# Kernel tuning notes

Measured on AMD Instinct MI355X. Metric: run time of the kernel, lower is better.

Reference implementation:

```python
import jax, jax.numpy as jnp
import numpy as np

N = 100_000      # nodes
E = 1_600_000    # nonzeros of the rescaled Laplacian (avg degree 16)
F_IN = 128
F_OUT = 128
K = 4


def setup_inputs() -> dict:
    key = jax.random.key(0)
    ks = jax.random.split(key, 6)
    x = jax.random.normal(ks[0], (N, F_IN), dtype=jnp.float32)
    filter_coeff = jax.random.normal(ks[1], (K, N), dtype=jnp.float32)
    # glorot-ish scale for [K, F_in, F_out]
    stdv = float(np.sqrt(6.0 / (F_IN + F_OUT)))
    weight = jax.random.uniform(ks[2], (K, F_IN, F_OUT), dtype=jnp.float32,
                                minval=-stdv, maxval=stdv)
    bias = jnp.zeros((F_OUT,), dtype=jnp.float32)
    src = jax.random.randint(ks[3], (E,), 0, N, dtype=jnp.int32)
    dst = jax.random.randint(ks[4], (E,), 0, N, dtype=jnp.int32)
    # edge values of L_hat = 2L/lambda_max - I (precomputed sparse matrix)
    edge_w = jax.random.normal(ks[5], (E,), dtype=jnp.float32) * 0.1
    return {"x": x, "filter_coeff": filter_coeff, "weight": weight,
            "bias": bias, "edge_w": edge_w, "src": src, "dst": dst}


def reference(x, filter_coeff, weight, bias, edge_w, src, dst):
    n = x.shape[0]

    def spmm(h):  # edge-weighted gather-scale-segment_sum == dgl.update_all
        return jax.ops.segment_sum(h[src] * edge_w[:, None], dst,
                                   num_segments=n)

    # Chebyshev recurrence: T0 = x, T1 = L_hat x, T_k = 2 L_hat T_{k-1} - T_{k-2}
    Tx0 = x
    out = (filter_coeff[0][:, None] * Tx0) @ weight[0]
    Tx1 = spmm(x)
    out = out + (filter_coeff[1][:, None] * Tx1) @ weight[1]
    for k in range(2, weight.shape[0]):
        Tx2 = 2.0 * spmm(Tx1) - Tx0
        out = out + (filter_coeff[k][:, None] * Tx2) @ weight[k]
        Tx0, Tx1 = Tx1, Tx2
    return out + bias
```

## Files before the change

kernel.cpp:

```cpp
#include <hip/hip_runtime.h>
#include <hip/hip_bf16.h>
#include <cstdio>

#define F 128
#define BSHIFT 9
#define BROWS 512
#define C2 4096

typedef __attribute__((ext_vector_type(4))) float f32x4;
typedef __attribute__((ext_vector_type(4))) unsigned short u16x4;
typedef __attribute__((ext_vector_type(8))) short s16x8;

__device__ inline unsigned short f2bf(float x) {
  unsigned int u = __float_as_uint(x);
  u += 0x7fffu + ((u >> 16) & 1u);
  return (unsigned short)(u >> 16);
}
__device__ inline float bf2f(unsigned int h) {
  return __uint_as_float(h << 16);
}

__global__ void bucket_hist_kernel(const int* __restrict__ dst, int* __restrict__ bhist,
                                   int E, int B) {
  __shared__ int h[256];
  int t = threadIdx.x;
  h[t] = 0;
  __syncthreads();
  for (int e = blockIdx.x * blockDim.x + t; e < E; e += gridDim.x * blockDim.x)
    atomicAdd(&h[dst[e] >> BSHIFT], 1);
  __syncthreads();
  if (t < B && h[t]) atomicAdd(&bhist[t], h[t]);
}

__global__ void bucket_scan_kernel(const int* __restrict__ bhist, int* __restrict__ bbase,
                                   int* __restrict__ bcursor, int* __restrict__ rp,
                                   int E, int B, int N) {
  __shared__ int sm[256];
  int t = threadIdx.x;
  int v = (t < B) ? bhist[t] : 0;
  sm[t] = v;
  __syncthreads();
  int x = v;
  for (int off = 1; off < 256; off <<= 1) {
    int add = (t >= off) ? sm[t - off] : 0;
    __syncthreads();
    x += add;
    sm[t] = x;
    __syncthreads();
  }
  int excl = x - v;
  if (t < B) { bbase[t] = excl; bcursor[t] = excl; }
  if (t == 0) { bbase[B] = E; rp[N] = E; }
}

__global__ __launch_bounds__(256) void bucket_scatter_kernel(
    const int* __restrict__ src, const int* __restrict__ dst, const float* __restrict__ ew,
    int* __restrict__ bcursor, unsigned int* __restrict__ stg_p, float* __restrict__ stg_w,
    int E, int B) {
  __shared__ int hist[256], gbase[256], cur[256], sm[256], scn[256];
  __shared__ unsigned int sp[C2];
  __shared__ float swt[C2];
  __shared__ int sdest[C2];
  int t = threadIdx.x;
  int e0 = blockIdx.x * C2;
  int cnt = min(C2, E - e0);
  hist[t] = 0;
  __syncthreads();
#pragma unroll
  for (int i = 0; i < C2 / 256; ++i) {
    int e = e0 + t + i * 256;
    if (e < E) atomicAdd(&hist[dst[e] >> BSHIFT], 1);
  }
  __syncthreads();
  int v = hist[t];
  gbase[t] = (t < B && v) ? atomicAdd(&bcursor[t], v) : 0;
  sm[t] = v;
  __syncthreads();
  int x = v;
  for (int off = 1; off < 256; off <<= 1) {
    int add = (t >= off) ? sm[t - off] : 0;
    __syncthreads();
    x += add;
    sm[t] = x;
    __syncthreads();
  }
  scn[t] = x - v;
  cur[t] = 0;
  __syncthreads();
#pragma unroll
  for (int i = 0; i < C2 / 256; ++i) {
    int e = e0 + t + i * 256;
    if (e < E) {
      int d = dst[e];
      int b = d >> BSHIFT;
      int r = atomicAdd(&cur[b], 1);
      int slot = scn[b] + r;
      sp[slot] = (unsigned int)src[e] | ((unsigned int)(d & (BROWS - 1)) << 17);
      swt[slot] = ew[e];
      sdest[slot] = gbase[b] + r;
    }
  }
  __syncthreads();
#pragma unroll
  for (int i = 0; i < C2 / 256; ++i) {
    int s = t + i * 256;
    if (s < cnt) {
      int dpos = sdest[s];
      stg_p[dpos] = sp[s];
      stg_w[dpos] = swt[s];
    }
  }
}

__global__ __launch_bounds__(256) void csr_build_kernel(
    const unsigned int* __restrict__ stg_p, const float* __restrict__ stg_w,
    const int* __restrict__ bbase, int* __restrict__ rp, int2* __restrict__ csr,
    int N, int B) {
  __shared__ int rhist[BROWS], rloc[BROWS], curp[BROWS];
  __shared__ int sm[256];
  int b = blockIdx.x, t = threadIdx.x;
  int row0 = b << BSHIFT;
  int base = bbase[b];
  int cnt = bbase[b + 1] - base;
  rhist[t] = 0;
  rhist[t + 256] = 0;
  __syncthreads();
  for (int s = base + t; s < base + cnt; s += 256)
    atomicAdd(&rhist[stg_p[s] >> 17], 1);
  __syncthreads();
  int a0 = rhist[2 * t], a1 = rhist[2 * t + 1];
  int pv = a0 + a1;
  sm[t] = pv;
  __syncthreads();
  int x = pv;
  for (int off = 1; off < 256; off <<= 1) {
    int add = (t >= off) ? sm[t - off] : 0;
    __syncthreads();
    x += add;
    sm[t] = x;
    __syncthreads();
  }
  int pexcl = x - pv;
  int r0 = 2 * t, r1 = 2 * t + 1;
  rloc[r0] = pexcl;
  rloc[r1] = pexcl + a0;
  if (row0 + r0 < N) rp[row0 + r0] = base + rloc[r0];
  if (row0 + r1 < N) rp[row0 + r1] = base + rloc[r1];
  curp[r0] = base + rloc[r0];
  curp[r1] = base + rloc[r1];
  __syncthreads();
  for (int s = base + t; s < base + cnt; s += 256) {
    unsigned int p = stg_p[s];
    int dl = p >> 17;
    int pos = atomicAdd(&curp[dl], 1);
    int2 entry;
    entry.x = (int)(p & 0x1ffffu);
    entry.y = __float_as_int(stg_w[s]);
    csr[pos] = entry;
  }
}

__global__ void convx_kernel(const float* __restrict__ x, unsigned short* __restrict__ xbf,
                             int total4) {
  int i = blockIdx.x * 256 + threadIdx.x;
  if (i >= total4) return;
  f32x4 v = ((const f32x4*)x)[i];
  u16x4 o;
  o.x = f2bf(v.x); o.y = f2bf(v.y); o.z = f2bf(v.z); o.w = f2bf(v.w);
  ((u16x4*)xbf)[i] = o;
}

__global__ __launch_bounds__(256) void spmm_kernel(
    const unsigned short* __restrict__ Tin, const unsigned short* __restrict__ Tsub,
    unsigned short* __restrict__ Tout, const int* __restrict__ rp,
    const int2* __restrict__ csr, int n, float scale) {
  int wv = blockIdx.x * (blockDim.x >> 6) + (threadIdx.x >> 6);
  if (wv >= n) return;
  int lane = threadIdx.x & 63;
  int sl = lane & 15;
  int eo = lane >> 4;
  int j0 = rp[wv], end = rp[wv + 1];
  const uint4* Tin4 = (const uint4*)Tin;
  float acc[8];
#pragma unroll
  for (int c = 0; c < 8; ++c) acc[c] = 0.f;

  for (int j = j0; j < end; j += 16) {
    int2 e[4];
    float w[4];
    uint4 v[4];
#pragma unroll
    for (int u = 0; u < 4; ++u) {
      int je = j + 4 * u + eo;
      bool live = je < end;
      e[u] = csr[live ? je : end - 1];
      w[u] = live ? __int_as_float(e[u].y) : 0.f;
    }
#pragma unroll
    for (int u = 0; u < 4; ++u) v[u] = Tin4[(size_t)e[u].x * 16 + sl];
#pragma unroll
    for (int u = 0; u < 4; ++u) {
      acc[0] = fmaf(w[u], bf2f(v[u].x & 0xffffu), acc[0]);
      acc[1] = fmaf(w[u], bf2f(v[u].x >> 16), acc[1]);
      acc[2] = fmaf(w[u], bf2f(v[u].y & 0xffffu), acc[2]);
      acc[3] = fmaf(w[u], bf2f(v[u].y >> 16), acc[3]);
      acc[4] = fmaf(w[u], bf2f(v[u].z & 0xffffu), acc[4]);
      acc[5] = fmaf(w[u], bf2f(v[u].z >> 16), acc[5]);
      acc[6] = fmaf(w[u], bf2f(v[u].w & 0xffffu), acc[6]);
      acc[7] = fmaf(w[u], bf2f(v[u].w >> 16), acc[7]);
    }
  }
#pragma unroll
  for (int h = 16; h <= 32; h <<= 1)
#pragma unroll
    for (int c = 0; c < 8; ++c) acc[c] += __shfl_xor(acc[c], h, 64);

  if (eo == 0) {
    float r[8];
#pragma unroll
    for (int c = 0; c < 8; ++c) r[c] = scale * acc[c];
    if (Tsub) {
      uint4 p = ((const uint4*)Tsub)[(size_t)wv * 16 + sl];
      r[0] -= bf2f(p.x & 0xffffu); r[1] -= bf2f(p.x >> 16);
      r[2] -= bf2f(p.y & 0xffffu); r[3] -= bf2f(p.y >> 16);
      r[4] -= bf2f(p.z & 0xffffu); r[5] -= bf2f(p.z >> 16);
      r[6] -= bf2f(p.w & 0xffffu); r[7] -= bf2f(p.w >> 16);
    }
    uint4 o;
    o.x = (unsigned)f2bf(r[0]) | ((unsigned)f2bf(r[1]) << 16);
    o.y = (unsigned)f2bf(r[2]) | ((unsigned)f2bf(r[3]) << 16);
    o.z = (unsigned)f2bf(r[4]) | ((unsigned)f2bf(r[5]) << 16);
    o.w = (unsigned)f2bf(r[6]) | ((unsigned)f2bf(r[7]) << 16);
    ((uint4*)Tout)[(size_t)wv * 16 + sl] = o;
  }
}

__global__ void convw_kernel(const float* __restrict__ W, unsigned short* __restrict__ Wt,
                             int total, int Kd) {
  int idx = blockIdx.x * 256 + threadIdx.x;
  if (idx >= total) return;
  int nn = idx / Kd;
  int rem = idx - nn * Kd;
  int kk = rem >> 7;
  int r = rem & 127;
  Wt[idx] = f2bf(W[(size_t)kk * F * F + (size_t)r * F + nn]);
}

struct GemmArgs {
  const unsigned short* A[8];
  const float* fc;
  const unsigned short* Wt;
  const float* bias;
  float* out;
  int n;
  int kslices;
};

__global__ __launch_bounds__(256) void gemm_kernel(GemmArgs args) {
  __shared__ __align__(16) unsigned short lds_a[128][72];
  __shared__ __align__(16) unsigned short lds_b[128][72];
  const int t = threadIdx.x;
  const int lane = t & 63;
  const int wid = t >> 6;
  const int wrow = wid >> 1, wcol = wid & 1;
  const int bm = blockIdx.x * 128;
  const int n = args.n;
  const int kiters = args.kslices * 2;
  const int pitchW = args.kslices * 128;

  const int srow = t >> 4;
  const int scol = (t & 15) * 4;

  f32x4 acc[4][4];
#pragma unroll
  for (int a = 0; a < 4; ++a)
#pragma unroll
    for (int b = 0; b < 4; ++b) acc[a][b] = (f32x4){0.f, 0.f, 0.f, 0.f};

  for (int it = 0; it < kiters; ++it) {
    __syncthreads();
    const int ks = it >> 1;
    const unsigned short* As = args.A[ks];
    const float* fcs = args.fc + (size_t)ks * n;
    const int cbase = (it & 1) * 64 + scol;
#pragma unroll
    for (int i = 0; i < 8; ++i) {
      int r = srow + 16 * i;
      int rg = bm + r;
      int rc = rg < n ? rg : n - 1;
      u16x4 v = *(const u16x4*)(As + (size_t)rc * F + cbase);
      float f = fcs[rc];
      u16x4 sv;
      sv.x = f2bf(bf2f(v.x) * f);
      sv.y = f2bf(bf2f(v.y) * f);
      sv.z = f2bf(bf2f(v.z) * f);
      sv.w = f2bf(bf2f(v.w) * f);
      *(u16x4*)&lds_a[r][scol] = sv;
    }
    {
      const unsigned short* Ws = args.Wt + it * 64;
#pragma unroll
      for (int i = 0; i < 8; ++i) {
        int r = srow + 16 * i;
        u16x4 w = *(const u16x4*)(Ws + (size_t)r * pitchW + scol);
        *(u16x4*)&lds_b[r][scol] = w;
      }
    }
    __syncthreads();
#pragma unroll
    for (int kk = 0; kk < 2; ++kk) {
      s16x8 af[4], bfr[4];
#pragma unroll
      for (int mt = 0; mt < 4; ++mt)
        af[mt] = *(const s16x8*)&lds_a[wrow * 64 + mt * 16 + (lane & 15)][kk * 32 + (lane >> 4) * 8];
#pragma unroll
      for (int nt = 0; nt < 4; ++nt)
        bfr[nt] = *(const s16x8*)&lds_b[wcol * 64 + nt * 16 + (lane & 15)][kk * 32 + (lane >> 4) * 8];
#pragma unroll
      for (int mt = 0; mt < 4; ++mt)
#pragma unroll
        for (int nt = 0; nt < 4; ++nt)
          acc[mt][nt] = __builtin_amdgcn_mfma_f32_16x16x32_bf16(af[mt], bfr[nt], acc[mt][nt], 0, 0, 0);
    }
  }

#pragma unroll
  for (int nt = 0; nt < 4; ++nt) {
    int col = wcol * 64 + nt * 16 + (lane & 15);
    float bv = args.bias[col];
#pragma unroll
    for (int mt = 0; mt < 4; ++mt) {
#pragma unroll
      for (int r4 = 0; r4 < 4; ++r4) {
        int row = bm + wrow * 64 + mt * 16 + (lane >> 4) * 4 + r4;
        if (row < n) args.out[(size_t)row * F + col] = acc[mt][nt][r4] + bv;
      }
    }
  }
}

extern "C" void kernel_launch(void* const* d_in, const int* in_sizes, int n_in,
                              void* d_out, int out_size, void* d_ws, size_t ws_size,
                              hipStream_t stream) {
  const float* x    = (const float*)d_in[0];
  const float* fc   = (const float*)d_in[1];
  const float* W    = (const float*)d_in[2];
  const float* bias = (const float*)d_in[3];
  const float* ew   = (const float*)d_in[4];
  const int*   src  = (const int*)d_in[5];
  const int*   dst  = (const int*)d_in[6];

  const int N = in_sizes[0] / F;
  const int K = in_sizes[2] / (F * F);
  const int E = in_sizes[4];
  const int B = (N + BROWS - 1) >> BSHIFT;

  size_t off = 0;
  char* base = (char*)d_ws;
  auto alloc = [&](size_t bytes) -> void* {
    void* p = base + off;
    off += (bytes + 511) & ~(size_t)511;
    return p;
  };
  int* rp              = (int*)alloc(((size_t)N + 1) * 4);
  int* bhist           = (int*)alloc(1024);
  int* bbase           = (int*)alloc(1040);
  int* bcursor         = (int*)alloc(1024);
  int2* csr            = (int2*)alloc((size_t)E * 8);
  unsigned short* Wt   = (unsigned short*)alloc((size_t)K * F * F * 2);
  unsigned short* xbf  = (unsigned short*)alloc((size_t)N * F * 2);
  unsigned short* T[8];
  T[0] = xbf;
  for (int k = 1; k < K && k < 8; ++k) T[k] = (unsigned short*)alloc((size_t)N * F * 2);
  unsigned int* stg_p;
  float* stg_w;
  if (K >= 3 && (size_t)N * F * 2 >= (size_t)E * 8) {
    stg_p = (unsigned int*)T[2];
    stg_w = (float*)(T[2] + (size_t)E * 2);
  } else {
    stg_p = (unsigned int*)alloc((size_t)E * 4);
    stg_w = (float*)alloc((size_t)E * 4);
  }
  if (off > ws_size) {
    fprintf(stderr, "kernel_launch: ws too small: need %zu have %zu\n", off, ws_size);
    return;
  }

  hipMemsetAsync(bhist, 0, 1024, stream);
  int hblocks = (E + 255) / 256;
  if (hblocks > 2048) hblocks = 2048;
  hipLaunchKernelGGL(bucket_hist_kernel, dim3(hblocks), dim3(256), 0, stream, dst, bhist, E, B);
  hipLaunchKernelGGL(bucket_scan_kernel, dim3(1), dim3(256), 0, stream, bhist, bbase, bcursor,
                     rp, E, B, N);
  int sblocks = (E + C2 - 1) / C2;
  hipLaunchKernelGGL(bucket_scatter_kernel, dim3(sblocks), dim3(256), 0, stream, src, dst, ew,
                     bcursor, stg_p, stg_w, E, B);
  hipLaunchKernelGGL(csr_build_kernel, dim3(B), dim3(256), 0, stream, stg_p, stg_w, bbase,
                     rp, csr, N, B);

  int total4 = N * F / 4;
  hipLaunchKernelGGL(convx_kernel, dim3((total4 + 255) / 256), dim3(256), 0, stream,
                     x, xbf, total4);

  int sb = (N + 3) / 4;
  if (K > 1)
    hipLaunchKernelGGL(spmm_kernel, dim3(sb), dim3(256), 0, stream, xbf,
                       (const unsigned short*)nullptr, T[1], rp, csr, N, 1.0f);
  for (int k = 2; k < K; ++k) {
    const unsigned short* prev = T[k - 2];
    hipLaunchKernelGGL(spmm_kernel, dim3(sb), dim3(256), 0, stream, T[k - 1], prev, T[k],
                       rp, csr, N, 2.0f);
  }

  int total = K * F * F;
  hipLaunchKernelGGL(convw_kernel, dim3((total + 255) / 256), dim3(256), 0, stream, W, Wt,
                     total, K * F);

  GemmArgs ga;
  for (int k = 0; k < 8; ++k) ga.A[k] = (k < K) ? T[k] : xbf;
  ga.fc = fc; ga.Wt = Wt; ga.bias = bias;
  ga.out = (float*)d_out;
  ga.n = N; ga.kslices = K;
  hipLaunchKernelGGL(gemm_kernel, dim3((N + 127) / 128), dim3(256), 0, stream, ga);
}
```

Measured before the change: 354.3 us.

## Double-buffer GEMM A tiles via async global-to-LDS loads, apply filter coeff post-MFMA

Restructures the final GEMM kernel so each k-slice's full 128x128 bf16 A tile is loaded straight into XOR-swizzled LDS with global_load_lds, double-buffered so the next slice loads while the current one runs on MFMA. Weights are read directly from global memory into registers rather than staged through LDS. The per-row filter coefficient is now applied to the fp32 partial products after each slice instead of rescaling A in bf16 before the multiply. This removes the per-element convert-scale-convert work and the synchronous staging. In exchange it uses more LDS and registers (launch bounds now target 2 blocks per unit) and slightly changes rounding.

```diff
diff --git a/kernel.cpp b/kernel.cpp
--- a/kernel.cpp
+++ b/kernel.cpp
@@ -18,6 +18,12 @@
 }
 __device__ inline float bf2f(unsigned int h) {
   return __uint_as_float(h << 16);
+}
+
+__device__ inline void async_load16(const void* g, void* l) {
+  __builtin_amdgcn_global_load_lds(
+      (const __attribute__((address_space(1))) void*)g,
+      (__attribute__((address_space(3))) void*)l, 16, 0, 0);
 }
 
 __global__ void bucket_hist_kernel(const int* __restrict__ dst, int* __restrict__ bhist,
@@ -256,72 +262,109 @@
   int kslices;
 };
 
-__global__ __launch_bounds__(256) void gemm_kernel(GemmArgs args) {
-  __shared__ __align__(16) unsigned short lds_a[128][72];
-  __shared__ __align__(16) unsigned short lds_b[128][72];
+__global__ __launch_bounds__(256, 2) void gemm_kernel(GemmArgs args) {
+  __shared__ __align__(16) unsigned short Alds[2][128 * 128];
+  __shared__ float fcT[8][128];
   const int t = threadIdx.x;
   const int lane = t & 63;
   const int wid = t >> 6;
   const int wrow = wid >> 1, wcol = wid & 1;
   const int bm = blockIdx.x * 128;
   const int n = args.n;
-  const int kiters = args.kslices * 2;
-  const int pitchW = args.kslices * 128;
-
-  const int srow = t >> 4;
-  const int scol = (t & 15) * 4;
-
-  f32x4 acc[4][4];
+  const int KS = args.kslices;
+  const int pitchW = KS * 128;
+
+  for (int i = t; i < KS * 128; i += 256) {
+    int k = i >> 7, r = i & 127;
+    int rg = bm + r;
+    if (rg >= n) rg = n - 1;
+    fcT[k][r] = args.fc[(size_t)k * n + rg];
+  }
+  asm volatile("s_waitcnt lgkmcnt(0)" ::: "memory");
+
+  const int rloc = lane >> 4;
+  const int uu = lane & 15;
+  auto stageA = [&](int ks, int b) {
+    const unsigned short* As = args.A[ks];
+#pragma unroll
+    for (int i = 0; i < 8; ++i) {
+      int c = wid * 8 + i;
+      int row = c * 4 + rloc;
+      int rg = bm + row;
+      if (rg >= n) rg = n - 1;
+      const void* g = (const void*)(As + (size_t)rg * F + (size_t)((uu ^ (row & 7)) << 3));
+      void* l = (void*)(&Alds[b][0] + c * 512);
+      async_load16(g, l);
+    }
+  };
+
+  f32x4 Cf[4][4];
 #pragma unroll
   for (int a = 0; a < 4; ++a)
 #pragma unroll
-    for (int b = 0; b < 4; ++b) acc[a][b] = (f32x4){0.f, 0.f, 0.f, 0.f};
-
-  for (int it = 0; it < kiters; ++it) {
-    __syncthreads();
-    const int ks = it >> 1;
-    const unsigned short* As = args.A[ks];
-    const float* fcs = args.fc + (size_t)ks * n;
-    const int cbase = (it & 1) * 64 + scol;
-#pragma unroll
-    for (int i = 0; i < 8; ++i) {
-      int r = srow + 16 * i;
-      int rg = bm + r;
-      int rc = rg < n ? rg : n - 1;
-      u16x4 v = *(const u16x4*)(As + (size_t)rc * F + cbase);
-      float f = fcs[rc];
-      u16x4 sv;
-      sv.x = f2bf(bf2f(v.x) * f);
-      sv.y = f2bf(bf2f(v.y) * f);
-      sv.z = f2bf(bf2f(v.z) * f);
-      sv.w = f2bf(bf2f(v.w) * f);
-      *(u16x4*)&lds_a[r][scol] = sv;
-    }
-    {
-      const unsigned short* Ws = args.Wt + it * 64;
-#pragma unroll
-      for (int i = 0; i < 8; ++i) {
-        int r = srow + 16 * i;
-        u16x4 w = *(const u16x4*)(Ws + (size_t)r * pitchW + scol);
-        *(u16x4*)&lds_b[r][scol] = w;
+    for (int bq = 0; bq < 4; ++bq) Cf[a][bq] = (f32x4){0.f, 0.f, 0.f, 0.f};
+
+  stageA(0, 0);
+
+  const int arow_b = wrow * 64 + (lane & 15);
+  const int brow_b = wcol * 64 + (lane & 15);
+  const int ke = lane >> 4;
+
+  for (int ks = 0; ks < KS; ++ks) {
+    const int b = ks & 1;
+
+    s16x8 bfr[4][4];
+    const unsigned short* Wb = args.Wt + (size_t)brow_b * pitchW + ks * 128 + ke * 8;
+#pragma unroll
+    for (int nt = 0; nt < 4; ++nt)
+#pragma unroll
+      for (int kk = 0; kk < 4; ++kk)
+        bfr[nt][kk] = *(const s16x8*)(Wb + (size_t)(nt * 16) * pitchW + kk * 32);
+
+    if (ks + 1 < KS) {
+      stageA(ks + 1, b ^ 1);
+      asm volatile("s_waitcnt vmcnt(8)" ::: "memory");
+    } else {
+      asm volatile("s_waitcnt vmcnt(0)" ::: "memory");
+    }
+    __builtin_amdgcn_sched_barrier(0);
+    __builtin_amdgcn_s_barrier();
+    __builtin_amdgcn_sched_barrier(0);
+
+    f32x4 acc[4][4];
+#pragma unroll
+    for (int a = 0; a < 4; ++a)
+#pragma unroll
+      for (int bq = 0; bq < 4; ++bq) acc[a][bq] = (f32x4){0.f, 0.f, 0.f, 0.f};
+
+#pragma unroll
+    for (int kk = 0; kk < 4; ++kk) {
+      s16x8 afr[4];
+#pragma unroll
+      for (int mt = 0; mt < 4; ++mt) {
+        int row = arow_b + mt * 16;
+        int unit = (kk * 4 + ke) ^ (row & 7);
+        afr[mt] = *(const s16x8*)&Alds[b][row * F + (unit << 3)];
       }
-    }
-    __syncthreads();
-#pragma unroll
-    for (int kk = 0; kk < 2; ++kk) {
-      s16x8 af[4], bfr[4];
 #pragma unroll
       for (int mt = 0; mt < 4; ++mt)
-        af[mt] = *(const s16x8*)&lds_a[wrow * 64 + mt * 16 + (lane & 15)][kk * 32 + (lane >> 4) * 8];
+#pragma unroll
+        for (int nt = 0; nt < 4; ++nt)
+          acc[mt][nt] = __builtin_amdgcn_mfma_f32_16x16x32_bf16(afr[mt], bfr[nt][kk],
+                                                                acc[mt][nt], 0, 0, 0);
+    }
+
+#pragma unroll
+    for (int mt = 0; mt < 4; ++mt) {
+      f32x4 fv = *(const f32x4*)&fcT[ks][wrow * 64 + mt * 16 + (lane >> 4) * 4];
 #pragma unroll
       for (int nt = 0; nt < 4; ++nt)
-        bfr[nt] = *(const s16x8*)&lds_b[wcol * 64 + nt * 16 + (lane & 15)][kk * 32 + (lane >> 4) * 8];
-#pragma unroll
-      for (int mt = 0; mt < 4; ++mt)
-#pragma unroll
-        for (int nt = 0; nt < 4; ++nt)
-          acc[mt][nt] = __builtin_amdgcn_mfma_f32_16x16x32_bf16(af[mt], bfr[nt], acc[mt][nt], 0, 0, 0);
-    }
+        Cf[mt][nt] += fv * acc[mt][nt];
+    }
+
+    __builtin_amdgcn_sched_barrier(0);
+    __builtin_amdgcn_s_barrier();
+    __builtin_amdgcn_sched_barrier(0);
   }
 
 #pragma unroll
@@ -333,7 +376,7 @@
 #pragma unroll
       for (int r4 = 0; r4 < 4; ++r4) {
         int row = bm + wrow * 64 + mt * 16 + (lane >> 4) * 4 + r4;
-        if (row < n) args.out[(size_t)row * F + col] = acc[mt][nt][r4] + bv;
+        if (row < n) args.out[(size_t)row * F + col] = Cf[mt][nt][r4] + bv;
       }
     }
   }
```

Measured after the change: 360.6 us. Within noise of the previous version (+1.8%).

## Drop LDS staging in GEMM; apply filter coefficients post-MFMA per K-slice

Applied to the files above, without the earlier changes.

The GEMM no longer stages A and W tiles through shared memory with barriers. Each wave computes a 32x128 output block, loading A fragments directly from global memory and W from a pre-permuted fragment-order layout built by convw_kernel. The per-row filter coefficient is applied to the fp32 partial product of each Chebyshev slice instead of rescaling bf16 inputs, which removes per-element conversions and a rounding step. The cost is more accumulator registers (two sets of 16 fragments) and uncoalesced direct global loads for A.

```diff
diff --git a/kernel.cpp b/kernel.cpp
--- a/kernel.cpp
+++ b/kernel.cpp
@@ -235,15 +235,18 @@
   }
 }
 
-__global__ void convw_kernel(const float* __restrict__ W, unsigned short* __restrict__ Wt,
-                             int total, int Kd) {
+__global__ void convw_kernel(const float* __restrict__ W, unsigned short* __restrict__ Wf,
+                             int total) {
   int idx = blockIdx.x * 256 + threadIdx.x;
   if (idx >= total) return;
-  int nn = idx / Kd;
-  int rem = idx - nn * Kd;
-  int kk = rem >> 7;
-  int r = rem & 127;
-  Wt[idx] = f2bf(W[(size_t)kk * F * F + (size_t)r * F + nn]);
+  int j = idx & 7;
+  int lane = (idx >> 3) & 63;
+  int nt = (idx >> 9) & 7;
+  int kk = (idx >> 12) & 3;
+  int ks = idx >> 14;
+  int kl = kk * 32 + (lane >> 4) * 8 + j;
+  int col = nt * 16 + (lane & 15);
+  Wf[idx] = f2bf(W[(size_t)ks * F * F + (size_t)kl * F + col]);
 }
 
 struct GemmArgs {
@@ -257,83 +260,83 @@
 };
 
 __global__ __launch_bounds__(256) void gemm_kernel(GemmArgs args) {
-  __shared__ __align__(16) unsigned short lds_a[128][72];
-  __shared__ __align__(16) unsigned short lds_b[128][72];
   const int t = threadIdx.x;
   const int lane = t & 63;
-  const int wid = t >> 6;
-  const int wrow = wid >> 1, wcol = wid & 1;
-  const int bm = blockIdx.x * 128;
+  const int w = t >> 6;
   const int n = args.n;
-  const int kiters = args.kslices * 2;
-  const int pitchW = args.kslices * 128;
-
-  const int srow = t >> 4;
-  const int scol = (t & 15) * 4;
-
-  f32x4 acc[4][4];
-#pragma unroll
-  for (int a = 0; a < 4; ++a)
-#pragma unroll
-    for (int b = 0; b < 4; ++b) acc[a][b] = (f32x4){0.f, 0.f, 0.f, 0.f};
-
-  for (int it = 0; it < kiters; ++it) {
-    __syncthreads();
-    const int ks = it >> 1;
+  const int r0 = blockIdx.x * 128 + w * 32;
+  if (r0 >= n) return;
+  const int arow = lane & 15;
+  const int kg = lane >> 4;
+
+  f32x4 Cf[2][8];
+#pragma unroll
+  for (int mt = 0; mt < 2; ++mt)
+#pragma unroll
+    for (int nt = 0; nt < 8; ++nt) Cf[mt][nt] = (f32x4){0.f, 0.f, 0.f, 0.f};
+
+  int row_a[2];
+#pragma unroll
+  for (int mt = 0; mt < 2; ++mt) {
+    int r = r0 + mt * 16 + arow;
+    row_a[mt] = r < n ? r : n - 1;
+  }
+
+  for (int ks = 0; ks < args.kslices; ++ks) {
     const unsigned short* As = args.A[ks];
-    const float* fcs = args.fc + (size_t)ks * n;
-    const int cbase = (it & 1) * 64 + scol;
-#pragma unroll
-    for (int i = 0; i < 8; ++i) {
-      int r = srow + 16 * i;
-      int rg = bm + r;
-      int rc = rg < n ? rg : n - 1;
-      u16x4 v = *(const u16x4*)(As + (size_t)rc * F + cbase);
-      float f = fcs[rc];
-      u16x4 sv;
-      sv.x = f2bf(bf2f(v.x) * f);
-      sv.y = f2bf(bf2f(v.y) * f);
-      sv.z = f2bf(bf2f(v.z) * f);
-      sv.w = f2bf(bf2f(v.w) * f);
-      *(u16x4*)&lds_a[r][scol] = sv;
-    }
-    {
-      const unsigned short* Ws = args.Wt + it * 64;
-#pragma unroll
-      for (int i = 0; i < 8; ++i) {
-        int r = srow + 16 * i;
-        u16x4 w = *(const u16x4*)(Ws + (size_t)r * pitchW + scol);
-        *(u16x4*)&lds_b[r][scol] = w;
+    const unsigned short* Wfb = args.Wt + (size_t)ks * 16384 + lane * 8;
+    f32x4 acc[2][8];
+#pragma unroll
+    for (int mt = 0; mt < 2; ++mt)
+#pragma unroll
+      for (int nt = 0; nt < 8; ++nt) acc[mt][nt] = (f32x4){0.f, 0.f, 0.f, 0.f};
+
+#pragma unroll
+    for (int kk = 0; kk < 4; ++kk) {
+      s16x8 af[2], bfr[8];
+#pragma unroll
+      for (int mt = 0; mt < 2; ++mt)
+        af[mt] = *(const s16x8*)(As + (size_t)row_a[mt] * F + kk * 32 + kg * 8);
+#pragma unroll
+      for (int nt = 0; nt < 8; ++nt)
+        bfr[nt] = *(const s16x8*)(Wfb + (kk * 8 + nt) * 512);
+#pragma unroll
+      for (int mt = 0; mt < 2; ++mt)
+#pragma unroll
+        for (int nt = 0; nt < 8; ++nt)
+          acc[mt][nt] = __builtin_amdgcn_mfma_f32_16x16x32_bf16(af[mt], bfr[nt],
+                                                                acc[mt][nt], 0, 0, 0);
+    }
+
+#pragma unroll
+    for (int mt = 0; mt < 2; ++mt) {
+      int row = r0 + mt * 16 + kg * 4;
+      f32x4 fv;
+      if (row + 3 < n) {
+        fv = *(const f32x4*)(args.fc + (size_t)ks * n + row);
+      } else {
+#pragma unroll
+        for (int r4 = 0; r4 < 4; ++r4) {
+          int rr = row + r4;
+          if (rr >= n) rr = n - 1;
+          fv[r4] = args.fc[(size_t)ks * n + rr];
+        }
       }
-    }
-    __syncthreads();
-#pragma unroll
-    for (int kk = 0; kk < 2; ++kk) {
-      s16x8 af[4], bfr[4];
-#pragma unroll
-      for (int mt = 0; mt < 4; ++mt)
-        af[mt] = *(const s16x8*)&lds_a[wrow * 64 + mt * 16 + (lane & 15)][kk * 32 + (lane >> 4) * 8];
-#pragma unroll
-      for (int nt = 0; nt < 4; ++nt)
-        bfr[nt] = *(const s16x8*)&lds_b[wcol * 64 + nt * 16 + (lane & 15)][kk * 32 + (lane >> 4) * 8];
-#pragma unroll
-      for (int mt = 0; mt < 4; ++mt)
-#pragma unroll
-        for (int nt = 0; nt < 4; ++nt)
-          acc[mt][nt] = __builtin_amdgcn_mfma_f32_16x16x32_bf16(af[mt], bfr[nt], acc[mt][nt], 0, 0, 0);
-    }
-  }
-
-#pragma unroll
-  for (int nt = 0; nt < 4; ++nt) {
-    int col = wcol * 64 + nt * 16 + (lane & 15);
+#pragma unroll
+      for (int nt = 0; nt < 8; ++nt) Cf[mt][nt] += fv * acc[mt][nt];
+    }
+  }
+
+#pragma unroll
+  for (int nt = 0; nt < 8; ++nt) {
+    int col = nt * 16 + arow;
     float bv = args.bias[col];
 #pragma unroll
-    for (int mt = 0; mt < 4; ++mt) {
+    for (int mt = 0; mt < 2; ++mt) {
 #pragma unroll
       for (int r4 = 0; r4 < 4; ++r4) {
-        int row = bm + wrow * 64 + mt * 16 + (lane >> 4) * 4 + r4;
-        if (row < n) args.out[(size_t)row * F + col] = acc[mt][nt][r4] + bv;
+        int row = r0 + mt * 16 + kg * 4 + r4;
+        if (row < n) args.out[(size_t)row * F + col] = Cf[mt][nt][r4] + bv;
       }
     }
   }
@@ -414,7 +417,7 @@
 
   int total = K * F * F;
   hipLaunchKernelGGL(convw_kernel, dim3((total + 255) / 256), dim3(256), 0, stream, W, Wt,
-                     total, K * F);
+                     total);
 
   GemmArgs ga;
   for (int k = 0; k < 8; ++k) ga.A[k] = (k < K) ? T[k] : xbf;
```

Result: no change. 354.7 us (+0.1%).
